# Optimization experiments

Hardware: AMD Instinct MI355X
Metric: run time of the kernel (lower is better)

## Reference

```python
import jax, jax.numpy as jnp
import numpy as np

# Polynomial structure (constants of the module, carried by `polynomial` in __init__)
MUL = 64                      # channel multiplicity
LS = [0, 1, 2]                # irrep degrees for both node features and sh
DIMS = [2 * l + 1 for l in LS]  # [1, 3, 5]
OFF = [0, 1, 4, 9]            # cumulative offsets of irrep dims within one channel-major block
X_SIZE = MUL * OFF[-1]        # 576
PATHS = [(l1, l2, l3) for l1 in LS for l2 in LS for l3 in LS
         if abs(l1 - l2) <= l3 <= l1 + l2]  # 15 CG-allowed paths
_rng = np.random.RandomState(0)
CG = {p: jnp.asarray((_rng.randn(2 * p[0] + 1, 2 * p[1] + 1, 2 * p[2] + 1) / 3.0).astype(np.float32))
      for p in PATHS}

N_NODES, N_EDGES = 20000, 320000


def setup_inputs() -> dict:
    key = jax.random.key(0)
    k1, k2, k3, k4 = jax.random.split(key, 4)
    x = jax.random.normal(k1, (N_NODES, X_SIZE), dtype=jnp.float32)
    sh = jax.random.normal(k2, (N_EDGES, OFF[-1]), dtype=jnp.float32)
    src = jax.random.randint(k3, (N_EDGES,), 0, N_NODES)
    dst = jax.random.randint(k4, (N_EDGES,), 0, N_NODES)
    return {"x": x, "sh": sh, "src": src, "dst": dst}


def reference(x, sh, src, dst):
    # gather node features to edges (input_indices for input 0)
    xe = x[src]                                           # [E, 576]
    E = xe.shape[0]
    # split into irrep segments: [E, MUL, 2l+1]
    segs_x = [xe[:, MUL * OFF[s]:MUL * OFF[s + 1]].reshape(E, MUL, DIMS[s]) for s in range(len(LS))]
    segs_sh = [sh[:, OFF[s]:OFF[s + 1]] for s in range(len(LS))]
    out_segs = [jnp.zeros((E, MUL, DIMS[s]), dtype=x.dtype) for s in range(len(LS))]
    # one segmented tensor-product einsum per (op, stp) in polynomial.operations
    for (l1, l2, l3) in PATHS:
        out_segs[l3] = out_segs[l3] + jnp.einsum(
            'eui,ej,ijk->euk', segs_x[l1], segs_sh[l2], CG[(l1, l2, l3)])
    edge_out = jnp.concatenate([o.reshape(E, -1) for o in out_segs], axis=1)  # [E, 576]
    # scatter_add by output_indices (edge -> node)
    out = jax.ops.segment_sum(edge_out, dst, num_segments=x.shape[0])         # [N, 576]
    return out
```

## Files before the change

### kernel.cpp

```cpp
#include <hip/hip_runtime.h>

typedef unsigned int uint32;
typedef unsigned short u16t;
typedef float f4u __attribute__((ext_vector_type(4), aligned(4)));
typedef uint32 u2u __attribute__((ext_vector_type(2), aligned(4)));

struct MTS { unsigned int mt[624]; int mti; };

constexpr unsigned int mt_next(MTS& s){
  if (s.mti >= 624){
    for (int i = 0; i < 624; i++){
      unsigned int y = (s.mt[i] & 0x80000000u) | (s.mt[(i+1)%624] & 0x7fffffffu);
      unsigned int v = s.mt[(i+397)%624] ^ (y >> 1);
      if (y & 1u) v ^= 2567483615u;
      s.mt[i] = v;
    }
    s.mti = 0;
  }
  unsigned int y = s.mt[s.mti]; s.mti++;
  y ^= y >> 11;
  y ^= (y << 7)  & 2636928640u;
  y ^= (y << 15) & 4022730752u;
  y ^= y >> 18;
  return y;
}
constexpr double mt_dbl(MTS& s){
  unsigned int a = mt_next(s) >> 5;
  unsigned int b = mt_next(s) >> 6;
  return ((double)a * 67108864.0 + (double)b) / 9007199254740992.0;
}

constexpr int NPAIR = 308;
struct GenData {
  double r2[NPAIR], x1[NPAIR], x2[NPAIR];
  int g_of_t[729];
};

constexpr GenData make_gen(){
  GenData g{};
  for (int i = 0; i < 729; i++) g.g_of_t[i] = -1;
  MTS s{};
  {
    unsigned int sd = 0u;
    for (int p = 0; p < 624; p++){
      s.mt[p] = sd;
      sd = 1812433253u * (sd ^ (sd >> 30)) + (unsigned)p + 1u;
    }
    s.mti = 624;
  }
  for (int p = 0; p < NPAIR; p++){
    double a = 0.0, b = 0.0, r = 0.0;
    do {
      a = 2.0 * mt_dbl(s) - 1.0;
      b = 2.0 * mt_dbl(s) - 1.0;
      r = a*a + b*b;
    } while (r >= 1.0 || r == 0.0);
    g.r2[p] = r; g.x1[p] = a; g.x2[p] = b;
  }
  const int L1[15] = {0,0,0,1,1,1,1,1,1,2,2,2,2,2,2};
  const int L2[15] = {0,1,2,0,1,1,1,2,2,0,1,1,2,2,2};
  const int L3[15] = {0,1,2,1,0,1,2,1,2,2,1,2,0,1,2};
  const int OFF[3] = {0,1,4};
  int gi = 0;
  for (int p = 0; p < 15; p++){
    int d1 = 2*L1[p]+1, d2 = 2*L2[p]+1, d3 = 2*L3[p]+1;
    for (int i = 0; i < d1; i++)
      for (int j = 0; j < d2; j++)
        for (int k = 0; k < d3; k++)
          g.g_of_t[(OFF[L1[p]]+i)*81 + (OFF[L2[p]]+j)*9 + (OFF[L3[p]]+k)] = gi++;
  }
  return g;
}

constexpr GenData h_gd = make_gen();
__constant__ GenData c_gd = h_gd;

__device__ __forceinline__ u16t f2b(float f){
  uint32 u = __float_as_uint(f);
  u += 0x7fffu + ((u >> 16) & 1u);
  return (u16t)(u >> 16);
}

__global__ __launch_bounds__(256) void gen_T_kernel(float* __restrict__ T){
  int t = blockIdx.x * blockDim.x + threadIdx.x;
  if (t >= 729) return;
  int gi = c_gd.g_of_t[t];
  float v = 0.f;
  if (gi >= 0){
    int p = gi >> 1;
    double r2 = c_gd.r2[p];
    double f  = sqrt(-2.0 * log(r2) / r2);
    double xx = (gi & 1) ? c_gd.x1[p] : c_gd.x2[p];
    v = (float)((f * xx) / 3.0);
  }
  T[t] = v;
}

__global__ __launch_bounds__(256) void prep_kernel(
    float* __restrict__ T, const float* __restrict__ x,
    uint32* __restrict__ xb2, const int* __restrict__ dst,
    int* __restrict__ cnt, int* __restrict__ pos, int N, int E){
  int t = blockIdx.x * 256 + threadIdx.x;
  if (t < 729){
    int gi = c_gd.g_of_t[t];
    float v = 0.f;
    if (gi >= 0){
      int p = gi >> 1;
      double r2 = c_gd.r2[p];
      double f  = sqrt(-2.0 * log(r2) / r2);
      double xx = (gi & 1) ? c_gd.x1[p] : c_gd.x2[p];
      v = (float)((f * xx) / 3.0);
    }
    T[t] = v;
  }
  if (t < E) pos[t] = atomicAdd(&cnt[dst[t]], 1);
  if (t >= N * 64) return;
  const int n = t >> 6, c = t & 63;
  const float* xr = x + (size_t)n * 576;
  float v[9];
  v[0] = xr[c];
#pragma unroll
  for (int q = 0; q < 3; q++) v[1 + q] = xr[64 + 3*c + q];
#pragma unroll
  for (int q = 0; q < 5; q++) v[4 + q] = xr[256 + 5*c + q];
  uint32* d = xb2 + (size_t)n * 320 + c * 5;
  d[0] = (uint32)f2b(v[0]) | ((uint32)f2b(v[1]) << 16);
  d[1] = (uint32)f2b(v[2]) | ((uint32)f2b(v[3]) << 16);
  d[2] = (uint32)f2b(v[4]) | ((uint32)f2b(v[5]) << 16);
  d[3] = (uint32)f2b(v[6]) | ((uint32)f2b(v[7]) << 16);
  d[4] = (uint32)f2b(v[8]);
}

__global__ void scan_kernel(const int* __restrict__ cnt, int* __restrict__ start, int n){
  __shared__ int part[1024];
  int t = threadIdx.x;
  int ch = (n + 1023) >> 10;
  int b0 = t * ch;
  int sum = 0;
  for (int j = 0; j < ch; j++){ int i = b0 + j; if (i < n) sum += cnt[i]; }
  part[t] = sum;
  __syncthreads();
  for (int off = 1; off < 1024; off <<= 1){
    int v = 0;
    if (t >= off) v = part[t - off];
    __syncthreads();
    part[t] += v;
    __syncthreads();
  }
  int run = (t > 0) ? part[t-1] : 0;
  for (int j = 0; j < ch; j++){
    int i = b0 + j;
    if (i < n){ start[i] = run; run += cnt[i]; }
  }
  if (t == 1023) start[n] = part[1023];
}

__global__ __launch_bounds__(256) void fill_kernel(const int* __restrict__ dst,
                                                   const int* __restrict__ src,
                                                   const int* __restrict__ start,
                                                   const int* __restrict__ pos,
                                                   uint2* __restrict__ epair, int E){
  int e = blockIdx.x * 256 + threadIdx.x;
  if (e >= E) return;
  int p = start[dst[e]] + pos[e];
  epair[p] = make_uint2((uint32)src[e], (uint32)e);
}

__device__ __forceinline__ int rfl(uint32 v){
  return __builtin_amdgcn_readfirstlane((int)v);
}

template<int HALF>
__device__ __forceinline__ void load_x(const uint32* __restrict__ xb2, int sn, int lane,
                                       uint32 (&xa)[3]){
  constexpr int DW0 = HALF ? 2 : 0;
  const uint32* xp = xb2 + (size_t)sn * 320 + lane * 5 + DW0;
  u2u a = *reinterpret_cast<const u2u*>(xp);
  xa[0] = a[0]; xa[1] = a[1];
  if (HALF) xa[2] = xp[2]; else xa[2] = 0;
}

__device__ __forceinline__ void load_sh(const float* __restrict__ sh, int e, float (&sv)[9]){
  const float* sp = sh + (size_t)e * 9;
  f4u a = *reinterpret_cast<const f4u*>(sp);
  f4u b = *reinterpret_cast<const f4u*>(sp + 4);
  float c = sp[8];
  sv[0]=a[0]; sv[1]=a[1]; sv[2]=a[2]; sv[3]=a[3];
  sv[4]=b[0]; sv[5]=b[1]; sv[6]=b[2]; sv[7]=b[3];
  sv[8]=c;
}

template<int HALF>
__device__ __forceinline__ void accum_half(
    const uint32* __restrict__ xb2, const float* __restrict__ sh,
    const uint2* __restrict__ epair, int s0, int s1, int lane, float (&z)[45])
{
  constexpr int IB  = HALF ? 4 : 0;
  constexpr int IC  = HALF ? 5 : 4;
  constexpr int DW0 = HALF ? 2 : 0;

  if (s0 >= s1) return;
  const int last = s1 - 1;

  auto fma_block = [&](const uint32 (&xa)[3], const float (&sv)[9]){
#pragma unroll
    for (int li = 0; li < IC; ++li){
      const int v = IB + li;
      const uint32 d = xa[(v >> 1) - DW0];
      const float xi = (v & 1) ? __uint_as_float(d & 0xffff0000u)
                               : __uint_as_float(d << 16);
#pragma unroll
      for (int j = 0; j < 9; ++j)
        z[li*9 + j] = fmaf(xi, sv[j], z[li*9 + j]);
    }
  };
  auto clampi = [&](int v){ return (v <= last) ? v : last; };

  uint2 p;
  p = epair[s0];            const int snA = rfl(p.x), enA = rfl(p.y);
  p = epair[clampi(s0+1)];  const int snB = rfl(p.x), enB = rfl(p.y);
  p = epair[clampi(s0+2)];  const int snC = rfl(p.x), enC = rfl(p.y);
  p = epair[clampi(s0+3)];  int sn3 = rfl(p.x), en3 = rfl(p.y);
  p = epair[clampi(s0+4)];  int sn4 = rfl(p.x), en4 = rfl(p.y);
  p = epair[clampi(s0+5)];  int sn5 = rfl(p.x), en5 = rfl(p.y);

  uint32 xA[3], xB[3], xC[3];
  float shA[9], shB[9], shC[9];
  load_x<HALF>(xb2, snA, lane, xA);  load_sh(sh, enA, shA);
  load_x<HALF>(xb2, snB, lane, xB);  load_sh(sh, enB, shB);
  load_x<HALF>(xb2, snC, lane, xC);  load_sh(sh, enC, shC);

  int i = s0;
  while (i + 2 < s1){
    p = epair[clampi(i + 6)]; const int sn6 = rfl(p.x), en6 = rfl(p.y);
    p = epair[clampi(i + 7)]; const int sn7 = rfl(p.x), en7 = rfl(p.y);
    p = epair[clampi(i + 8)]; const int sn8 = rfl(p.x), en8 = rfl(p.y);

    fma_block(xA, shA);
    load_x<HALF>(xb2, sn3, lane, xA);  load_sh(sh, en3, shA);
    fma_block(xB, shB);
    load_x<HALF>(xb2, sn4, lane, xB);  load_sh(sh, en4, shB);
    fma_block(xC, shC);
    load_x<HALF>(xb2, sn5, lane, xC);  load_sh(sh, en5, shC);

    sn3 = sn6; en3 = en6; sn4 = sn7; en4 = en7; sn5 = sn8; en5 = en8;
    i += 3;
  }
  if (i < s1)     fma_block(xA, shA);
  if (i + 1 < s1) fma_block(xB, shB);
}

template<int HALF>
__device__ __forceinline__ void epilogue_half(const float* __restrict__ Tl,
                                              const float (&z)[45], float (&o)[9])
{
  constexpr int IB = HALF ? 4 : 0;
  constexpr int IC = HALF ? 5 : 4;
#pragma unroll
  for (int m = 0; m < IC * 9; ++m){
    const int t = IB * 9 + m;
    const float4 wa = *reinterpret_cast<const float4*>(&Tl[t*12]);
    const float4 wb = *reinterpret_cast<const float4*>(&Tl[t*12 + 4]);
    const float  w8 = Tl[t*12 + 8];
    const float  zt = z[m];
    o[0] = fmaf(zt, wa.x, o[0]);
    o[1] = fmaf(zt, wa.y, o[1]);
    o[2] = fmaf(zt, wa.z, o[2]);
    o[3] = fmaf(zt, wa.w, o[3]);
    o[4] = fmaf(zt, wb.x, o[4]);
    o[5] = fmaf(zt, wb.y, o[5]);
    o[6] = fmaf(zt, wb.z, o[6]);
    o[7] = fmaf(zt, wb.w, o[7]);
    o[8] = fmaf(zt, w8,   o[8]);
  }
}

__global__ __launch_bounds__(128, 5) void tp_fused(
    const uint32* __restrict__ xb2, const float* __restrict__ sh,
    const uint2* __restrict__ epair, const int* __restrict__ starts,
    const float* __restrict__ Tg, float* __restrict__ out, int n_nodes)
{
  __shared__ __align__(16) float Tl[81 * 12];
  __shared__ __align__(16) float red[64 * 13];

  for (int s = threadIdx.x; s < 81 * 12; s += 128){
    const int t = s / 12, k = s % 12;
    Tl[s] = (k < 9) ? Tg[t * 9 + k] : 0.f;
  }
  __syncthreads();

  const int half = threadIdx.x >> 6;
  const int lane = threadIdx.x & 63;
  const int node = blockIdx.x;

  const int s0 = rfl((uint32)starts[node]);
  const int s1 = rfl((uint32)starts[node + 1]);

  float z[45];
#pragma unroll
  for (int t = 0; t < 45; t++) z[t] = 0.f;

  float o[9];
#pragma unroll
  for (int k = 0; k < 9; k++) o[k] = 0.f;

  if (half == 0){
    accum_half<0>(xb2, sh, epair, s0, s1, lane, z);
    epilogue_half<0>(Tl, z, o);
    float* rp = &red[lane * 13];
    *reinterpret_cast<float4*>(rp)     = make_float4(o[0], o[1], o[2], o[3]);
    *reinterpret_cast<float4*>(rp + 4) = make_float4(o[4], o[5], o[6], o[7]);
    rp[8] = o[8];
  } else {
    accum_half<1>(xb2, sh, epair, s0, s1, lane, z);
    epilogue_half<1>(Tl, z, o);
  }

  __syncthreads();

  if (half == 1){
    const float* rp = &red[lane * 13];
    const float4 ra = *reinterpret_cast<const float4*>(rp);
    const float4 rb = *reinterpret_cast<const float4*>(rp + 4);
    const float  r8 = rp[8];
    o[0] += ra.x; o[1] += ra.y; o[2] += ra.z; o[3] += ra.w;
    o[4] += rb.x; o[5] += rb.y; o[6] += rb.z; o[7] += rb.w;
    o[8] += r8;

    float* orow = out + (size_t)node * 576;
    orow[lane] = o[0];
#pragma unroll
    for (int t = 0; t < 3; t++) orow[64 + 3*lane + t] = o[1 + t];
#pragma unroll
    for (int t = 0; t < 5; t++) orow[256 + 5*lane + t] = o[4 + t];
  }
}

__device__ __forceinline__ float bcast_lane(float v, int lane){
  return __uint_as_float(__builtin_amdgcn_readlane(__float_as_uint(v), lane));
}

__global__ __launch_bounds__(256) void tp_edge_atomic(
    const float* __restrict__ x, const float* __restrict__ sh,
    const int* __restrict__ src, const int* __restrict__ dst,
    const float* __restrict__ Tg, float* __restrict__ out, int E)
{
  const int wv = threadIdx.x >> 6;
  const int lane = threadIdx.x & 63;
  const int e = blockIdx.x * 4 + wv;
  if (e >= E) return;

  const int i0 = lane / 9, k0 = lane % 9;
  const bool has1 = (lane < 17);
  const int e1 = has1 ? (64 + lane) : 63;
  const int i1 = e1 / 9, k1 = e1 % 9;
  float t0[9], t1[9];
#pragma unroll
  for (int j = 0; j < 9; j++){
    t0[j] = Tg[i0*81 + j*9 + k0];
    t1[j] = Tg[i1*81 + j*9 + k1];
  }

  const int sn = src[e];
  const float* she = sh + (size_t)e * 9;
  float sv[9];
#pragma unroll
  for (int j = 0; j < 9; j++) sv[j] = she[j];

  float w0 = 0.f, w1 = 0.f;
#pragma unroll
  for (int j = 0; j < 9; j++) w0 = fmaf(sv[j], t0[j], w0);
#pragma unroll
  for (int j = 0; j < 9; j++) w1 = fmaf(sv[j], t1[j], w1);

  const float* xr = x + (size_t)sn * 576;
  float xv[9];
  xv[0] = xr[lane];
#pragma unroll
  for (int t = 0; t < 3; t++) xv[1 + t] = xr[64 + 3*lane + t];
#pragma unroll
  for (int t = 0; t < 5; t++) xv[4 + t] = xr[256 + 5*lane + t];

  float o[9];
#pragma unroll
  for (int k = 0; k < 9; k++) o[k] = 0.f;
#pragma unroll
  for (int i = 0; i < 9; i++){
    const float xi = xv[i];
#pragma unroll
    for (int k = 0; k < 9; k++){
      const int t = i*9 + k;
      const float w = (t < 64) ? bcast_lane(w0, t) : bcast_lane(w1, t - 64);
      o[k] = fmaf(xi, w, o[k]);
    }
  }

  float* orow = out + (size_t)dst[e] * 576;
  atomicAdd(&orow[lane], o[0]);
#pragma unroll
  for (int t = 0; t < 3; t++) atomicAdd(&orow[64 + 3*lane + t], o[1 + t]);
#pragma unroll
  for (int t = 0; t < 5; t++) atomicAdd(&orow[256 + 5*lane + t], o[4 + t]);
}

extern "C" void kernel_launch(void* const* d_in, const int* in_sizes, int n_in,
                              void* d_out, int out_size, void* d_ws, size_t ws_size,
                              hipStream_t stream)
{
  const float* x  = (const float*)d_in[0];
  const float* sh = (const float*)d_in[1];
  const int* src  = (const int*)d_in[2];
  const int* dst  = (const int*)d_in[3];
  float* out = (float*)d_out;

  const int N = in_sizes[0] / 576;
  const int E = in_sizes[2];

  const size_t o_cnt  = 1024;
  const size_t o_strt = o_cnt + (size_t)N;
  const size_t o_pos  = o_strt + (size_t)N + 1;
  size_t o_ep   = o_pos + (size_t)E;
  o_ep = (o_ep + 1) & ~(size_t)1;
  size_t o_xb   = o_ep + (size_t)2 * E;
  o_xb = (o_xb + 3) & ~(size_t)3;
  const size_t need = (o_xb + (size_t)320 * N) * 4;

  float* Tw = (float*)d_ws;

  if (ws_size >= need){
    int* cnt    = (int*)d_ws + o_cnt;
    int* strt   = (int*)d_ws + o_strt;
    int* pos    = (int*)d_ws + o_pos;
    uint2* ep   = (uint2*)((uint32*)d_ws + o_ep);
    uint32* xb2 = (uint32*)d_ws + o_xb;

    hipMemsetAsync(cnt, 0, (size_t)N * 4, stream);
    const int rh = (N * 64 > E ? N * 64 : E);
    prep_kernel<<<(rh + 255) / 256, 256, 0, stream>>>(Tw, x, xb2, dst, cnt, pos, N, E);
    scan_kernel<<<1, 1024, 0, stream>>>(cnt, strt, N);
    fill_kernel<<<(E + 255) / 256, 256, 0, stream>>>(dst, src, strt, pos, ep, E);
    tp_fused<<<N, 128, 0, stream>>>(xb2, sh, ep, strt, Tw, out, N);
  } else {
    gen_T_kernel<<<3, 256, 0, stream>>>(Tw);
    hipMemsetAsync(out, 0, (size_t)out_size * 4, stream);
    tp_edge_atomic<<<(E + 3) / 4, 256, 0, stream>>>(x, sh, src, dst, Tw, out, E);
  }
}
```

Before: 157.3 us.

## Gather fp32 node features directly and pack two nodes per block

Drops the bf16 pre-conversion of node features in the prep kernel, so the fused kernel gathers fp32 rows of x directly. This removes a full pass over x and the packed buffer, but doubles the bytes gathered per edge from node features, and the per-lane strided loads are no longer vectorized. It also changes the fused kernel to 256-thread blocks that each handle two nodes (two waves per node), with launch bounds adjusted accordingly. The last block clamps an out-of-range node index, so it redundantly recomputes and rewrites the final node.

```diff
diff --git a/kernel.cpp b/kernel.cpp
--- a/kernel.cpp
+++ b/kernel.cpp
@@ -1,9 +1,7 @@
 #include <hip/hip_runtime.h>
 
 typedef unsigned int uint32;
-typedef unsigned short u16t;
 typedef float f4u __attribute__((ext_vector_type(4), aligned(4)));
-typedef uint32 u2u __attribute__((ext_vector_type(2), aligned(4)));
 
 struct MTS { unsigned int mt[624]; int mti; };
 
@@ -75,31 +73,9 @@
 constexpr GenData h_gd = make_gen();
 __constant__ GenData c_gd = h_gd;
 
-__device__ __forceinline__ u16t f2b(float f){
-  uint32 u = __float_as_uint(f);
-  u += 0x7fffu + ((u >> 16) & 1u);
-  return (u16t)(u >> 16);
-}
-
-__global__ __launch_bounds__(256) void gen_T_kernel(float* __restrict__ T){
-  int t = blockIdx.x * blockDim.x + threadIdx.x;
-  if (t >= 729) return;
-  int gi = c_gd.g_of_t[t];
-  float v = 0.f;
-  if (gi >= 0){
-    int p = gi >> 1;
-    double r2 = c_gd.r2[p];
-    double f  = sqrt(-2.0 * log(r2) / r2);
-    double xx = (gi & 1) ? c_gd.x1[p] : c_gd.x2[p];
-    v = (float)((f * xx) / 3.0);
-  }
-  T[t] = v;
-}
-
 __global__ __launch_bounds__(256) void prep_kernel(
-    float* __restrict__ T, const float* __restrict__ x,
-    uint32* __restrict__ xb2, const int* __restrict__ dst,
-    int* __restrict__ cnt, int* __restrict__ pos, int N, int E){
+    float* __restrict__ T, const int* __restrict__ dst,
+    int* __restrict__ cnt, int* __restrict__ pos, int E){
   int t = blockIdx.x * 256 + threadIdx.x;
   if (t < 729){
     int gi = c_gd.g_of_t[t];
@@ -114,21 +90,6 @@
     T[t] = v;
   }
   if (t < E) pos[t] = atomicAdd(&cnt[dst[t]], 1);
-  if (t >= N * 64) return;
-  const int n = t >> 6, c = t & 63;
-  const float* xr = x + (size_t)n * 576;
-  float v[9];
-  v[0] = xr[c];
-#pragma unroll
-  for (int q = 0; q < 3; q++) v[1 + q] = xr[64 + 3*c + q];
-#pragma unroll
-  for (int q = 0; q < 5; q++) v[4 + q] = xr[256 + 5*c + q];
-  uint32* d = xb2 + (size_t)n * 320 + c * 5;
-  d[0] = (uint32)f2b(v[0]) | ((uint32)f2b(v[1]) << 16);
-  d[1] = (uint32)f2b(v[2]) | ((uint32)f2b(v[3]) << 16);
-  d[2] = (uint32)f2b(v[4]) | ((uint32)f2b(v[5]) << 16);
-  d[3] = (uint32)f2b(v[6]) | ((uint32)f2b(v[7]) << 16);
-  d[4] = (uint32)f2b(v[8]);
 }
 
 __global__ void scan_kernel(const int* __restrict__ cnt, int* __restrict__ start, int n){
@@ -171,13 +132,18 @@
 }
 
 template<int HALF>
-__device__ __forceinline__ void load_x(const uint32* __restrict__ xb2, int sn, int lane,
-                                       uint32 (&xa)[3]){
-  constexpr int DW0 = HALF ? 2 : 0;
-  const uint32* xp = xb2 + (size_t)sn * 320 + lane * 5 + DW0;
-  u2u a = *reinterpret_cast<const u2u*>(xp);
-  xa[0] = a[0]; xa[1] = a[1];
-  if (HALF) xa[2] = xp[2]; else xa[2] = 0;
+__device__ __forceinline__ void load_x(const float* __restrict__ x, int sn, int lane,
+                                       float (&xv)[5]){
+  const float* r = x + (size_t)sn * 576;
+  if (HALF == 0){
+    xv[0] = r[lane];
+    const float* b = r + 64 + 3*lane;
+    xv[1] = b[0]; xv[2] = b[1]; xv[3] = b[2];
+    xv[4] = 0.f;
+  } else {
+    const float* b = r + 256 + 5*lane;
+    xv[0] = b[0]; xv[1] = b[1]; xv[2] = b[2]; xv[3] = b[3]; xv[4] = b[4];
+  }
 }
 
 __device__ __forceinline__ void load_sh(const float* __restrict__ sh, int e, float (&sv)[9]){
@@ -192,23 +158,18 @@
 
 template<int HALF>
 __device__ __forceinline__ void accum_half(
-    const uint32* __restrict__ xb2, const float* __restrict__ sh,
+    const float* __restrict__ x, const float* __restrict__ sh,
     const uint2* __restrict__ epair, int s0, int s1, int lane, float (&z)[45])
 {
-  constexpr int IB  = HALF ? 4 : 0;
-  constexpr int IC  = HALF ? 5 : 4;
-  constexpr int DW0 = HALF ? 2 : 0;
+  constexpr int IC = HALF ? 5 : 4;
 
   if (s0 >= s1) return;
   const int last = s1 - 1;
 
-  auto fma_block = [&](const uint32 (&xa)[3], const float (&sv)[9]){
+  auto fma_block = [&](const float (&xv)[5], const float (&sv)[9]){
 #pragma unroll
     for (int li = 0; li < IC; ++li){
-      const int v = IB + li;
-      const uint32 d = xa[(v >> 1) - DW0];
-      const float xi = (v & 1) ? __uint_as_float(d & 0xffff0000u)
-                               : __uint_as_float(d << 16);
+      const float xi = xv[li];
 #pragma unroll
       for (int j = 0; j < 9; ++j)
         z[li*9 + j] = fmaf(xi, sv[j], z[li*9 + j]);
@@ -224,11 +185,11 @@
   p = epair[clampi(s0+4)];  int sn4 = rfl(p.x), en4 = rfl(p.y);
   p = epair[clampi(s0+5)];  int sn5 = rfl(p.x), en5 = rfl(p.y);
 
-  uint32 xA[3], xB[3], xC[3];
+  float xA[5], xB[5], xC[5];
   float shA[9], shB[9], shC[9];
-  load_x<HALF>(xb2, snA, lane, xA);  load_sh(sh, enA, shA);
-  load_x<HALF>(xb2, snB, lane, xB);  load_sh(sh, enB, shB);
-  load_x<HALF>(xb2, snC, lane, xC);  load_sh(sh, enC, shC);
+  load_x<HALF>(x, snA, lane, xA);  load_sh(sh, enA, shA);
+  load_x<HALF>(x, snB, lane, xB);  load_sh(sh, enB, shB);
+  load_x<HALF>(x, snC, lane, xC);  load_sh(sh, enC, shC);
 
   int i = s0;
   while (i + 2 < s1){
@@ -237,11 +198,11 @@
     p = epair[clampi(i + 8)]; const int sn8 = rfl(p.x), en8 = rfl(p.y);
 
     fma_block(xA, shA);
-    load_x<HALF>(xb2, sn3, lane, xA);  load_sh(sh, en3, shA);
+    load_x<HALF>(x, sn3, lane, xA);  load_sh(sh, en3, shA);
     fma_block(xB, shB);
-    load_x<HALF>(xb2, sn4, lane, xB);  load_sh(sh, en4, shB);
+    load_x<HALF>(x, sn4, lane, xB);  load_sh(sh, en4, shB);
     fma_block(xC, shC);
-    load_x<HALF>(xb2, sn5, lane, xC);  load_sh(sh, en5, shC);
+    load_x<HALF>(x, sn5, lane, xC);  load_sh(sh, en5, shC);
 
     sn3 = sn6; en3 = en6; sn4 = sn7; en4 = en7; sn5 = sn8; en5 = en8;
     i += 3;
@@ -275,23 +236,26 @@
   }
 }
 
-__global__ __launch_bounds__(128, 5) void tp_fused(
-    const uint32* __restrict__ xb2, const float* __restrict__ sh,
+__global__ __launch_bounds__(256, 4) void tp_fused(
+    const float* __restrict__ x, const float* __restrict__ sh,
     const uint2* __restrict__ epair, const int* __restrict__ starts,
     const float* __restrict__ Tg, float* __restrict__ out, int n_nodes)
 {
   __shared__ __align__(16) float Tl[81 * 12];
-  __shared__ __align__(16) float red[64 * 13];
-
-  for (int s = threadIdx.x; s < 81 * 12; s += 128){
+  __shared__ __align__(16) float red[2][64 * 13];
+
+  for (int s = threadIdx.x; s < 81 * 12; s += 256){
     const int t = s / 12, k = s % 12;
     Tl[s] = (k < 9) ? Tg[t * 9 + k] : 0.f;
   }
   __syncthreads();
 
-  const int half = threadIdx.x >> 6;
+  const int wv   = threadIdx.x >> 6;
   const int lane = threadIdx.x & 63;
-  const int node = blockIdx.x;
+  const int nib  = wv >> 1;
+  const int half = wv & 1;
+  int node = blockIdx.x * 2 + nib;
+  if (node >= n_nodes) node = n_nodes - 1;
 
   const int s0 = rfl((uint32)starts[node]);
   const int s1 = rfl((uint32)starts[node + 1]);
@@ -305,21 +269,21 @@
   for (int k = 0; k < 9; k++) o[k] = 0.f;
 
   if (half == 0){
-    accum_half<0>(xb2, sh, epair, s0, s1, lane, z);
+    accum_half<0>(x, sh, epair, s0, s1, lane, z);
     epilogue_half<0>(Tl, z, o);
-    float* rp = &red[lane * 13];
+    float* rp = &red[nib][lane * 13];
     *reinterpret_cast<float4*>(rp)     = make_float4(o[0], o[1], o[2], o[3]);
     *reinterpret_cast<float4*>(rp + 4) = make_float4(o[4], o[5], o[6], o[7]);
     rp[8] = o[8];
   } else {
-    accum_half<1>(xb2, sh, epair, s0, s1, lane, z);
+    accum_half<1>(x, sh, epair, s0, s1, lane, z);
     epilogue_half<1>(Tl, z, o);
   }
 
   __syncthreads();
 
   if (half == 1){
-    const float* rp = &red[lane * 13];
+    const float* rp = &red[nib][lane * 13];
     const float4 ra = *reinterpret_cast<const float4*>(rp);
     const float4 rb = *reinterpret_cast<const float4*>(rp + 4);
     const float  r8 = rp[8];
@@ -338,6 +302,21 @@
 
 __device__ __forceinline__ float bcast_lane(float v, int lane){
   return __uint_as_float(__builtin_amdgcn_readlane(__float_as_uint(v), lane));
+}
+
+__global__ __launch_bounds__(256) void gen_T_kernel(float* __restrict__ T){
+  int t = blockIdx.x * blockDim.x + threadIdx.x;
+  if (t >= 729) return;
+  int gi = c_gd.g_of_t[t];
+  float v = 0.f;
+  if (gi >= 0){
+    int p = gi >> 1;
+    double r2 = c_gd.r2[p];
+    double f  = sqrt(-2.0 * log(r2) / r2);
+    double xx = (gi & 1) ? c_gd.x1[p] : c_gd.x2[p];
+    v = (float)((f * xx) / 3.0);
+  }
+  T[t] = v;
 }
 
 __global__ __launch_bounds__(256) void tp_edge_atomic(
@@ -421,9 +400,7 @@
   const size_t o_pos  = o_strt + (size_t)N + 1;
   size_t o_ep   = o_pos + (size_t)E;
   o_ep = (o_ep + 1) & ~(size_t)1;
-  size_t o_xb   = o_ep + (size_t)2 * E;
-  o_xb = (o_xb + 3) & ~(size_t)3;
-  const size_t need = (o_xb + (size_t)320 * N) * 4;
+  const size_t need = (o_ep + (size_t)2 * E) * 4;
 
   float* Tw = (float*)d_ws;
 
@@ -432,14 +409,12 @@
     int* strt   = (int*)d_ws + o_strt;
     int* pos    = (int*)d_ws + o_pos;
     uint2* ep   = (uint2*)((uint32*)d_ws + o_ep);
-    uint32* xb2 = (uint32*)d_ws + o_xb;
 
     hipMemsetAsync(cnt, 0, (size_t)N * 4, stream);
-    const int rh = (N * 64 > E ? N * 64 : E);
-    prep_kernel<<<(rh + 255) / 256, 256, 0, stream>>>(Tw, x, xb2, dst, cnt, pos, N, E);
+    prep_kernel<<<(E + 255) / 256, 256, 0, stream>>>(Tw, dst, cnt, pos, E);
     scan_kernel<<<1, 1024, 0, stream>>>(cnt, strt, N);
     fill_kernel<<<(E + 255) / 256, 256, 0, stream>>>(dst, src, strt, pos, ep, E);
-    tp_fused<<<N, 128, 0, stream>>>(xb2, sh, ep, strt, Tw, out, N);
+    tp_fused<<<(N + 1) / 2, 256, 0, stream>>>(x, sh, ep, strt, Tw, out, N);
   } else {
     gen_T_kernel<<<3, 256, 0, stream>>>(Tw);
     hipMemsetAsync(out, 0, (size_t)out_size * 4, stream);
```

After: 173.5 us. 10.4% more time.

## Replace serial scan with atomic bucket allocation and pack two nodes per block

Applied to the files above, without the earlier changes.

The single-block 1024-thread prefix scan is replaced by a parallel kernel that gives each node's CSR segment an arbitrary offset through atomicAdd on a global counter. Segment end is now computed from start plus count, so starts need not be monotone. tp_fused now handles two nodes per 256-thread block, which halves the block count and spreads the shared T-table load across two nodes. The costs are a non-deterministic segment layout with less locality, and a duplicated write for the last node when N is odd (the duplicate block stores identical values).

```diff
diff --git a/kernel.cpp b/kernel.cpp
--- a/kernel.cpp
+++ b/kernel.cpp
@@ -131,28 +131,11 @@
   d[4] = (uint32)f2b(v[8]);
 }
 
-__global__ void scan_kernel(const int* __restrict__ cnt, int* __restrict__ start, int n){
-  __shared__ int part[1024];
-  int t = threadIdx.x;
-  int ch = (n + 1023) >> 10;
-  int b0 = t * ch;
-  int sum = 0;
-  for (int j = 0; j < ch; j++){ int i = b0 + j; if (i < n) sum += cnt[i]; }
-  part[t] = sum;
-  __syncthreads();
-  for (int off = 1; off < 1024; off <<= 1){
-    int v = 0;
-    if (t >= off) v = part[t - off];
-    __syncthreads();
-    part[t] += v;
-    __syncthreads();
-  }
-  int run = (t > 0) ? part[t-1] : 0;
-  for (int j = 0; j < ch; j++){
-    int i = b0 + j;
-    if (i < n){ start[i] = run; run += cnt[i]; }
-  }
-  if (t == 1023) start[n] = part[1023];
+__global__ __launch_bounds__(256) void alloc_kernel(const int* __restrict__ cnt,
+                                                    int* __restrict__ start,
+                                                    int* __restrict__ counter, int n){
+  int t = blockIdx.x * 256 + threadIdx.x;
+  if (t < n) start[t] = atomicAdd(counter, cnt[t]);
 }
 
 __global__ __launch_bounds__(256) void fill_kernel(const int* __restrict__ dst,
@@ -275,26 +258,30 @@
   }
 }
 
-__global__ __launch_bounds__(128, 5) void tp_fused(
+__global__ __launch_bounds__(256, 5) void tp_fused(
     const uint32* __restrict__ xb2, const float* __restrict__ sh,
     const uint2* __restrict__ epair, const int* __restrict__ starts,
-    const float* __restrict__ Tg, float* __restrict__ out, int n_nodes)
+    const int* __restrict__ cnt, const float* __restrict__ Tg,
+    float* __restrict__ out, int n_nodes)
 {
   __shared__ __align__(16) float Tl[81 * 12];
-  __shared__ __align__(16) float red[64 * 13];
-
-  for (int s = threadIdx.x; s < 81 * 12; s += 128){
+  __shared__ __align__(16) float red[2][64 * 13];
+
+  for (int s = threadIdx.x; s < 81 * 12; s += 256){
     const int t = s / 12, k = s % 12;
     Tl[s] = (k < 9) ? Tg[t * 9 + k] : 0.f;
   }
   __syncthreads();
 
-  const int half = threadIdx.x >> 6;
+  const int wv   = threadIdx.x >> 6;
   const int lane = threadIdx.x & 63;
-  const int node = blockIdx.x;
+  const int nib  = wv >> 1;
+  const int half = wv & 1;
+  int node = blockIdx.x * 2 + nib;
+  if (node >= n_nodes) node = n_nodes - 1;
 
   const int s0 = rfl((uint32)starts[node]);
-  const int s1 = rfl((uint32)starts[node + 1]);
+  const int s1 = s0 + rfl((uint32)cnt[node]);
 
   float z[45];
 #pragma unroll
@@ -307,7 +294,7 @@
   if (half == 0){
     accum_half<0>(xb2, sh, epair, s0, s1, lane, z);
     epilogue_half<0>(Tl, z, o);
-    float* rp = &red[lane * 13];
+    float* rp = &red[nib][lane * 13];
     *reinterpret_cast<float4*>(rp)     = make_float4(o[0], o[1], o[2], o[3]);
     *reinterpret_cast<float4*>(rp + 4) = make_float4(o[4], o[5], o[6], o[7]);
     rp[8] = o[8];
@@ -319,7 +306,7 @@
   __syncthreads();
 
   if (half == 1){
-    const float* rp = &red[lane * 13];
+    const float* rp = &red[nib][lane * 13];
     const float4 ra = *reinterpret_cast<const float4*>(rp);
     const float4 rb = *reinterpret_cast<const float4*>(rp + 4);
     const float  r8 = rp[8];
@@ -417,8 +404,9 @@
   const int E = in_sizes[2];
 
   const size_t o_cnt  = 1024;
-  const size_t o_strt = o_cnt + (size_t)N;
-  const size_t o_pos  = o_strt + (size_t)N + 1;
+  const size_t o_ctr  = o_cnt + (size_t)N;
+  const size_t o_strt = o_ctr + 1;
+  const size_t o_pos  = o_strt + (size_t)N;
   size_t o_ep   = o_pos + (size_t)E;
   o_ep = (o_ep + 1) & ~(size_t)1;
   size_t o_xb   = o_ep + (size_t)2 * E;
@@ -429,17 +417,18 @@
 
   if (ws_size >= need){
     int* cnt    = (int*)d_ws + o_cnt;
+    int* ctr    = (int*)d_ws + o_ctr;
     int* strt   = (int*)d_ws + o_strt;
     int* pos    = (int*)d_ws + o_pos;
     uint2* ep   = (uint2*)((uint32*)d_ws + o_ep);
     uint32* xb2 = (uint32*)d_ws + o_xb;
 
-    hipMemsetAsync(cnt, 0, (size_t)N * 4, stream);
+    hipMemsetAsync(cnt, 0, ((size_t)N + 1) * 4, stream);
     const int rh = (N * 64 > E ? N * 64 : E);
     prep_kernel<<<(rh + 255) / 256, 256, 0, stream>>>(Tw, x, xb2, dst, cnt, pos, N, E);
-    scan_kernel<<<1, 1024, 0, stream>>>(cnt, strt, N);
+    alloc_kernel<<<(N + 255) / 256, 256, 0, stream>>>(cnt, strt, ctr, N);
     fill_kernel<<<(E + 255) / 256, 256, 0, stream>>>(dst, src, strt, pos, ep, E);
-    tp_fused<<<N, 128, 0, stream>>>(xb2, sh, ep, strt, Tw, out, N);
+    tp_fused<<<(N + 1) / 2, 256, 0, stream>>>(xb2, sh, ep, strt, cnt, Tw, out, N);
   } else {
     gen_T_kernel<<<3, 256, 0, stream>>>(Tw);
     hipMemsetAsync(out, 0, (size_t)out_size * 4, stream);
```

Measured after the change: 133.3 us, median of 2. -15.2%, faster.
